# Optimization experiments

Hardware: AMD Instinct MI355X
Metric: run time of the kernel (lower is better)

The kernel has to match this reference:

```python
import jax, jax.numpy as jnp
import numpy as np

B, H, W = 64, 14, 14
DIM, NH, LORA = 768, 12, 4
HD = DIM // NH  # 64


def setup_inputs() -> dict:
    key = jax.random.key(0)
    ks = jax.random.split(key, 12)
    s = 0.02
    return {
        "x": jax.random.normal(ks[0], (B, H, W, DIM), dtype=jnp.float32),
        "qkv_w": jax.random.normal(ks[1], (3 * DIM, DIM), dtype=jnp.float32) * s,
        "qkv_b": jax.random.normal(ks[2], (3 * DIM,), dtype=jnp.float32) * s,
        "proj_w": jax.random.normal(ks[3], (DIM, DIM), dtype=jnp.float32) * s,
        "proj_b": jax.random.normal(ks[4], (DIM,), dtype=jnp.float32) * s,
        "la_q": jax.random.normal(ks[5], (LORA, DIM), dtype=jnp.float32) * s,
        "lb_q": jax.random.normal(ks[6], (DIM, LORA), dtype=jnp.float32) * s,
        "la_v": jax.random.normal(ks[7], (LORA, DIM), dtype=jnp.float32) * s,
        "lb_v": jax.random.normal(ks[8], (DIM, LORA), dtype=jnp.float32) * s,
        "rel_pos_h": jax.random.normal(ks[9], (2 * H - 1, HD), dtype=jnp.float32) * s,
        "rel_pos_w": jax.random.normal(ks[10], (2 * W - 1, HD), dtype=jnp.float32) * s,
    }


def reference(x, qkv_w, qkv_b, proj_w, proj_b, la_q, lb_q, la_v, lb_v, rel_pos_h, rel_pos_w):
    b, h, w, c = x.shape
    nh, hd = NH, c // NH
    scale = hd ** -0.5

    # qkv projection with LoRA deltas on q and v
    qkv = x @ qkv_w.T + qkv_b                       # (b,h,w,3c)
    new_q = (x @ la_q.T) @ lb_q.T                   # (b,h,w,c)
    new_v = (x @ la_v.T) @ lb_v.T
    qkv = qkv.at[..., :c].add(new_q)
    qkv = qkv.at[..., 2 * c:].add(new_v)

    qkv = qkv.reshape(b, h * w, 3, nh, hd).transpose(2, 0, 3, 1, 4)
    qkv = qkv.reshape(3, b * nh, h * w, hd)
    q, k, v = qkv[0], qkv[1], qkv[2]

    attn = jnp.einsum('bqd,bkd->bqk', q * scale, k)  # (b*nh, hw, hw)

    # decomposed relative position bias; q_size == k_size so no interpolation
    idx_h = jnp.arange(h)[:, None] - jnp.arange(h)[None, :] + (h - 1)
    idx_w = jnp.arange(w)[:, None] - jnp.arange(w)[None, :] + (w - 1)
    Rh = rel_pos_h[idx_h]                            # (h,h,hd)
    Rw = rel_pos_w[idx_w]                            # (w,w,hd)
    r_q = q.reshape(b * nh, h, w, hd)
    rel_h = jnp.einsum('bhwc,hkc->bhwk', r_q, Rh)    # (b*nh,h,w,h)
    rel_w = jnp.einsum('bhwc,wkc->bhwk', r_q, Rw)    # (b*nh,h,w,w)
    attn = (attn.reshape(b * nh, h, w, h, w)
            + rel_h[:, :, :, :, None]
            + rel_w[:, :, :, None, :]).reshape(b * nh, h * w, h * w)

    attn = jax.nn.softmax(attn, axis=-1)
    out = jnp.einsum('bqk,bkd->bqd', attn, v)        # (b*nh, hw, hd)
    out = out.reshape(b, nh, h, w, hd).transpose(0, 2, 3, 1, 4).reshape(b, h, w, c)
    return out @ proj_w.T + proj_b
```

## Files before the change

### kernel.cpp

```cpp
#include <hip/hip_runtime.h>
#include <stdint.h>

#define DIM   768
#define NH    12
#define HD    64
#define NT    196
#define M_ROWS 12544

typedef __attribute__((ext_vector_type(8))) short bf16x8;
typedef __attribute__((ext_vector_type(4))) float f32x4;

__device__ __forceinline__ float b2f(short s) {
  union { unsigned u; float f; } c;
  c.u = ((unsigned)(unsigned short)s) << 16;
  return c.f;
}
__device__ __forceinline__ short f2b(float f) {
  union { float f; unsigned u; } c; c.f = f;
  unsigned u = c.u;
  u += 0x7fffu + ((u >> 16) & 1u);
  return (short)(u >> 16);
}

__device__ __forceinline__ f32x4 mfma16(bf16x8 a, bf16x8 b, f32x4 c) {
  return __builtin_amdgcn_mfma_f32_16x16x32_bf16(a, b, c, 0, 0, 0);
}

__device__ __forceinline__ void g2lds16(const short* g, short* l) {
  __builtin_amdgcn_global_load_lds(
      (const __attribute__((address_space(1))) void*)g,
      (__attribute__((address_space(3))) void*)l, 16, 0, 0);
}

struct CvtArgs { const float* src[5]; int n4[5]; int off[5]; };

__global__ __launch_bounds__(256) void k_cvt(CvtArgs a, short* __restrict__ dst) {
  const int tid = blockIdx.x * 256 + threadIdx.x;
  const int stride = gridDim.x * 256;
  #pragma unroll
  for (int s = 0; s < 5; ++s) {
    const float4* sp = (const float4*)a.src[s];
    short4* dp = (short4*)(dst + a.off[s]);
    const int n4 = a.n4[s];
    for (int i = tid; i < n4; i += stride) {
      float4 v = sp[i];
      short4 o = { f2b(v.x), f2b(v.y), f2b(v.z), f2b(v.w) };
      dp[i] = o;
    }
  }
}

__global__ __launch_bounds__(256) void k_lora_xa(
    const float* __restrict__ x, const float* __restrict__ la_q,
    const float* __restrict__ la_v, float* __restrict__ xa)
{
  __shared__ float sla[8][DIM];
  const int tid = threadIdx.x;
  for (int i = tid; i < 8 * DIM; i += 256) {
    int j = i / DIM, c = i - j * DIM;
    sla[j][c] = (j < 4) ? la_q[j * DIM + c] : la_v[(j - 4) * DIM + c];
  }
  __syncthreads();
  const int lane = tid & 63, wid = tid >> 6;
  const int m = blockIdx.x * 4 + wid;
  const float4* xr = (const float4*)(x + (size_t)m * DIM);
  float s[8] = {};
  #pragma unroll
  for (int i = 0; i < 3; ++i) {
    float4 xv = xr[lane + 64 * i];
    int c = (lane + 64 * i) * 4;
    #pragma unroll
    for (int j = 0; j < 8; ++j)
      s[j] += xv.x * sla[j][c] + xv.y * sla[j][c + 1]
            + xv.z * sla[j][c + 2] + xv.w * sla[j][c + 3];
  }
  #pragma unroll
  for (int j = 0; j < 8; ++j) {
    #pragma unroll
    for (int off = 32; off; off >>= 1) s[j] += __shfl_xor(s[j], off);
  }
  if (lane == 0) {
    float* o = xa + m * 8;
    #pragma unroll
    for (int j = 0; j < 8; ++j) o[j] = s[j];
  }
}

template<int EPI>
__global__ __launch_bounds__(256) void k_gemm(
    const short* __restrict__ A, const short* __restrict__ B,
    const float* __restrict__ bias, const float* __restrict__ xa,
    const float* __restrict__ lb_q, const float* __restrict__ lb_v,
    short* __restrict__ out, float* __restrict__ outf)
{
  constexpr int K = DIM;
  __shared__ short sA[128 * 32];
  __shared__ short sB[128 * 32];
  const int tid = threadIdx.x, lane = tid & 63, wid = tid >> 6;
  const int rm0 = blockIdx.x * 128, cn0 = blockIdx.y * 128;
  const int wm = (wid >> 1) * 64, wn = (wid & 1) * 64;
  const int fr = lane & 15, fg = lane >> 4;
  f32x4 acc[4][4] = {};
  const short* ga = A + (size_t)(rm0 + (tid >> 2)) * K + (tid & 3) * 8;
  const short* gb = B + (size_t)(cn0 + (tid >> 2)) * K + (tid & 3) * 8;
  short* lA = sA + wid * 512;
  short* lB = sB + wid * 512;

  for (int kt = 0; kt < K; kt += 32) {
    g2lds16(ga + kt, lA);
    g2lds16(ga + 64 * K + kt, lA + 2048);
    g2lds16(gb + kt, lB);
    g2lds16(gb + 64 * K + kt, lB + 2048);
    __syncthreads();
    bf16x8 af[4], bg[4];
    #pragma unroll
    for (int i = 0; i < 4; ++i)
      af[i] = *(const bf16x8*)&sA[(wm + i * 16 + fr) * 32 + fg * 8];
    #pragma unroll
    for (int j = 0; j < 4; ++j)
      bg[j] = *(const bf16x8*)&sB[(wn + j * 16 + fr) * 32 + fg * 8];
    #pragma unroll
    for (int i = 0; i < 4; ++i)
      #pragma unroll
      for (int j = 0; j < 4; ++j)
        acc[i][j] = mfma16(af[i], bg[j], acc[i][j]);
    __syncthreads();
  }

  int ncol[4]; float biasv[4];
  #pragma unroll
  for (int j = 0; j < 4; ++j) {
    ncol[j] = cn0 + wn + j * 16 + fr;
    biasv[j] = bias[ncol[j]];
  }

  if (EPI == 0) {
    const int reg = cn0 / DIM;
    float lb[4][4];
    if (reg != 1) {
      const float* lbt = (reg == 0) ? lb_q : lb_v;
      #pragma unroll
      for (int j = 0; j < 4; ++j) {
        int ni = ncol[j] - reg * DIM;
        #pragma unroll
        for (int l = 0; l < 4; ++l) lb[j][l] = lbt[ni * 4 + l];
      }
    }
    #pragma unroll
    for (int i = 0; i < 4; ++i) {
      #pragma unroll
      for (int r = 0; r < 4; ++r) {
        int m = rm0 + wm + i * 16 + fg * 4 + r;
        int b_i = m / NT, p = m - b_i * NT;
        float xv0 = 0, xv1 = 0, xv2 = 0, xv3 = 0;
        if (reg != 1) {
          const float* xp = xa + m * 8 + (reg == 2 ? 4 : 0);
          xv0 = xp[0]; xv1 = xp[1]; xv2 = xp[2]; xv3 = xp[3];
        }
        #pragma unroll
        for (int j = 0; j < 4; ++j) {
          float val = acc[i][j][r] + biasv[j];
          if (reg != 1)
            val += xv0 * lb[j][0] + xv1 * lb[j][1] + xv2 * lb[j][2] + xv3 * lb[j][3];
          int ni = ncol[j] - reg * DIM;
          int head = ni >> 6, d = ni & 63;
          out[(size_t)reg * (M_ROWS * DIM)
              + ((size_t)(b_i * NH + head) * NT + p) * HD + d] = f2b(val);
        }
      }
    }
  } else {
    #pragma unroll
    for (int i = 0; i < 4; ++i)
      #pragma unroll
      for (int r = 0; r < 4; ++r) {
        int m = rm0 + wm + i * 16 + fg * 4 + r;
        #pragma unroll
        for (int j = 0; j < 4; ++j)
          outf[(size_t)m * DIM + ncol[j]] = acc[i][j][r] + biasv[j];
      }
  }
}

__global__ __launch_bounds__(256) void k_attn(
    const short* __restrict__ qb, const short* __restrict__ kb,
    const short* __restrict__ vb, const short* __restrict__ rph,
    const short* __restrict__ rpw, short* __restrict__ ao)
{
  __shared__ short vst[64][216];
  __shared__ short pwb[4][16][208];
  __shared__ short relh[NT * 14];
  __shared__ short relw[NT * 14];
  const int tid = threadIdx.x, lane = tid & 63, wid = tid >> 6;
  const int fr = lane & 15, fg = lane >> 4;
  const int bh = blockIdx.x;
  const int b_i = bh / NH, head = bh - b_i * NH;
  const short* q0 = qb + (size_t)bh * NT * HD;
  const short* k0 = kb + (size_t)bh * NT * HD;
  const short* v0 = vb + (size_t)bh * NT * HD;

  for (int i = tid; i < 64 * 20; i += 256) {
    int d = i / 20, c = 196 + (i - (i / 20) * 20);
    vst[d][c] = 0;
  }
  for (int t = tid; t < NT * 8; t += 256) {
    int p = t >> 3, d0 = (t & 7) * 8;
    bf16x8 vv = *(const bf16x8*)(v0 + p * HD + d0);
    #pragma unroll
    for (int j = 0; j < 8; ++j) vst[d0 + j][p] = vv[j];
  }
  for (int job = wid; job < 28; job += 4) {
    const int isW = job >= 14 ? 1 : 0;
    const int fx = isW ? job - 14 : job;
    const int qrow = isW ? fr * 14 + fx : fx * 14 + fr;
    const bool aok = fr < 14;
    const short* rp = isW ? rpw : rph;
    int ridx = fx - fr + 13;
    ridx = ridx < 0 ? 0 : (ridx > 26 ? 26 : ridx);
    f32x4 racc = {0.f, 0.f, 0.f, 0.f};
    #pragma unroll
    for (int ks = 0; ks < 2; ++ks) {
      bf16x8 afr = {0,0,0,0,0,0,0,0};
      if (aok) afr = *(const bf16x8*)(q0 + qrow * HD + ks * 32 + fg * 8);
      bf16x8 bfr = *(const bf16x8*)(rp + ridx * HD + ks * 32 + fg * 8);
      racc = mfma16(afr, bfr, racc);
    }
    #pragma unroll
    for (int r = 0; r < 4; ++r) {
      int rr = fg * 4 + r;
      if (rr < 14 && fr < 14) {
        int p = isW ? rr * 14 + fx : fx * 14 + rr;
        (isW ? relw : relh)[p * 14 + fr] = f2b(racc[r]);
      }
    }
  }
  __syncthreads();

  const float scale = 0.125f;
  for (int t = wid; t < 13; t += 4) {
    const int m0 = t * 16;
    bf16x8 aq0 = {0,0,0,0,0,0,0,0}, aq1 = {0,0,0,0,0,0,0,0};
    {
      int arow = m0 + fr;
      if (arow < NT) {
        aq0 = *(const bf16x8*)(q0 + arow * HD + fg * 8);
        aq1 = *(const bf16x8*)(q0 + arow * HD + 32 + fg * 8);
      }
    }
    f32x4 sc[13] = {};
    #pragma unroll
    for (int ct = 0; ct < 13; ++ct) {
      int brow = ct * 16 + fr;
      bf16x8 bk0 = {0,0,0,0,0,0,0,0}, bk1 = {0,0,0,0,0,0,0,0};
      if (brow < NT) {
        bk0 = *(const bf16x8*)(k0 + brow * HD + fg * 8);
        bk1 = *(const bf16x8*)(k0 + brow * HD + 32 + fg * 8);
      }
      sc[ct] = mfma16(aq0, bk0, sc[ct]);
      sc[ct] = mfma16(aq1, bk1, sc[ct]);
    }
    float rmax[4] = {-1e30f, -1e30f, -1e30f, -1e30f};
    #pragma unroll
    for (int ct = 0; ct < 13; ++ct) {
      int kk = ct * 16 + fr;
      int kh = kk / 14, kw = kk - kh * 14;
      #pragma unroll
      for (int r = 0; r < 4; ++r) {
        int p = m0 + fg * 4 + r;
        float v;
        if (kk < NT && p < NT)
          v = sc[ct][r] * scale + b2f(relh[p * 14 + kh]) + b2f(relw[p * 14 + kw]);
        else
          v = -1e30f;
        sc[ct][r] = v;
        rmax[r] = fmaxf(rmax[r], v);
      }
    }
    #pragma unroll
    for (int r = 0; r < 4; ++r) {
      rmax[r] = fmaxf(rmax[r], __shfl_xor(rmax[r], 1));
      rmax[r] = fmaxf(rmax[r], __shfl_xor(rmax[r], 2));
      rmax[r] = fmaxf(rmax[r], __shfl_xor(rmax[r], 4));
      rmax[r] = fmaxf(rmax[r], __shfl_xor(rmax[r], 8));
    }
    float rsum[4] = {0.f, 0.f, 0.f, 0.f};
    #pragma unroll
    for (int ct = 0; ct < 13; ++ct)
      #pragma unroll
      for (int r = 0; r < 4; ++r) {
        float e = __expf(sc[ct][r] - rmax[r]);
        sc[ct][r] = e;
        rsum[r] += e;
      }
    #pragma unroll
    for (int r = 0; r < 4; ++r) {
      rsum[r] += __shfl_xor(rsum[r], 1);
      rsum[r] += __shfl_xor(rsum[r], 2);
      rsum[r] += __shfl_xor(rsum[r], 4);
      rsum[r] += __shfl_xor(rsum[r], 8);
    }
    #pragma unroll
    for (int ct = 0; ct < 13; ++ct)
      #pragma unroll
      for (int r = 0; r < 4; ++r)
        pwb[wid][fg * 4 + r][ct * 16 + fr] = f2b(sc[ct][r]);

    f32x4 oacc[4] = {};
    #pragma unroll
    for (int ks = 0; ks < 7; ++ks) {
      const bool hi = (ks == 6) && (fg >= 2);
      bf16x8 pa = {0,0,0,0,0,0,0,0};
      if (!hi) pa = *(const bf16x8*)&pwb[wid][fr][ks * 32 + fg * 8];
      #pragma unroll
      for (int dt = 0; dt < 4; ++dt) {
        bf16x8 vv = {0,0,0,0,0,0,0,0};
        if (!hi) vv = *(const bf16x8*)&vst[dt * 16 + fr][ks * 32 + fg * 8];
        oacc[dt] = mfma16(pa, vv, oacc[dt]);
      }
    }
    #pragma unroll
    for (int r = 0; r < 4; ++r) {
      int p = m0 + fg * 4 + r;
      if (p < NT) {
        float inv = 1.0f / rsum[r];
        size_t base = ((size_t)(b_i * NT + p)) * DIM + head * HD;
        #pragma unroll
        for (int dt = 0; dt < 4; ++dt)
          ao[base + dt * 16 + fr] = f2b(oacc[dt][r] * inv);
      }
    }
  }
}

extern "C" void kernel_launch(void* const* d_in, const int* in_sizes, int n_in,
                              void* d_out, int out_size, void* d_ws, size_t ws_size,
                              hipStream_t stream) {
  const float *x = nullptr, *qkv_w = nullptr, *qkv_b = nullptr,
              *proj_w = nullptr, *proj_b = nullptr, *rph = nullptr,
              *rpw = nullptr;
  const float* c3072[4] = {nullptr, nullptr, nullptr, nullptr};
  int n3072 = 0, n1728 = 0;
  for (int i = 0; i < n_in; ++i) {
    const float* p = (const float*)d_in[i];
    switch (in_sizes[i]) {
      case 9633792: x = p; break;
      case 1769472: qkv_w = p; break;
      case 2304:    qkv_b = p; break;
      case 589824:  proj_w = p; break;
      case 768:     proj_b = p; break;
      case 3072:    if (n3072 < 4) c3072[n3072++] = p; break;
      case 1728:    { if (n1728 == 0) rph = p; else rpw = p; ++n1728; } break;
      default: break;
    }
  }
  const bool alpha = (n_in >= 1 && in_sizes[n_in - 1] == 9633792);
  const float* la_q = c3072[0];
  const float* lb_q = alpha ? c3072[2] : c3072[1];
  const float* la_v = alpha ? c3072[1] : c3072[2];
  const float* lb_v = c3072[3];

  float* out = (float*)d_out;

  char* ws = (char*)d_ws;
  float* xa   = (float*)ws;
  short* qkvb = (short*)(ws + 401408);
  short* q_   = qkvb;
  short* k_   = qkvb + (size_t)M_ROWS * DIM;
  short* v_   = qkvb + (size_t)2 * M_ROWS * DIM;
  short* cvt  = (short*)(ws + 401408 + 57802752);
  short* xb      = cvt;
  short* qkv_wb  = cvt + 9633792;
  short* proj_wb = cvt + 11403264;
  short* rphb    = cvt + 11993088;
  short* rpwb    = cvt + 11994816;
  short* ao = xb;

  CvtArgs ca;
  ca.src[0] = x;      ca.n4[0] = 9633792 / 4;  ca.off[0] = 0;
  ca.src[1] = qkv_w;  ca.n4[1] = 1769472 / 4;  ca.off[1] = 9633792;
  ca.src[2] = proj_w; ca.n4[2] =  589824 / 4;  ca.off[2] = 11403264;
  ca.src[3] = rph;    ca.n4[3] =    1728 / 4;  ca.off[3] = 11993088;
  ca.src[4] = rpw;    ca.n4[4] =    1728 / 4;  ca.off[4] = 11994816;

  k_cvt<<<1024, 256, 0, stream>>>(ca, cvt);
  k_lora_xa<<<3136, 256, 0, stream>>>(x, la_q, la_v, xa);
  k_gemm<0><<<dim3(98, 18), 256, 0, stream>>>(xb, qkv_wb, qkv_b, xa, lb_q, lb_v,
                                              qkvb, nullptr);
  k_attn<<<768, 256, 0, stream>>>(q_, k_, v_, rphb, rpwb, ao);
  k_gemm<1><<<dim3(98, 6), 256, 0, stream>>>(ao, proj_wb, proj_b, nullptr, nullptr,
                                             nullptr, nullptr, out);
}
```

Measured before the change: 206.7 us.

## Fuse x bf16 conversion into LoRA kernel, swizzle GEMM LDS, remap blocks per XCD

The fp32-to-bf16 conversion of x now happens inside the LoRA down-projection kernel, which already reads every row of x, so x is read from global memory once instead of twice. The GEMM kernels get an XOR swizzle on the LDS layout (applied on both the global-to-LDS writes and the fragment reads) to reduce bank conflicts. They also use a 1D grid remapped so consecutive output tiles land on the same XCD for better L2 reuse. The weight conversion kernel shrinks to four sources and 512 blocks.

Measured after the change: 193.4 us. -6.4%, faster.

```diff
diff --git a/kernel.cpp b/kernel.cpp
--- a/kernel.cpp
+++ b/kernel.cpp
@@ -32,13 +32,13 @@
       (__attribute__((address_space(3))) void*)l, 16, 0, 0);
 }
 
-struct CvtArgs { const float* src[5]; int n4[5]; int off[5]; };
+struct CvtArgs { const float* src[4]; int n4[4]; int off[4]; };
 
 __global__ __launch_bounds__(256) void k_cvt(CvtArgs a, short* __restrict__ dst) {
   const int tid = blockIdx.x * 256 + threadIdx.x;
   const int stride = gridDim.x * 256;
   #pragma unroll
-  for (int s = 0; s < 5; ++s) {
+  for (int s = 0; s < 4; ++s) {
     const float4* sp = (const float4*)a.src[s];
     short4* dp = (short4*)(dst + a.off[s]);
     const int n4 = a.n4[s];
@@ -52,7 +52,8 @@
 
 __global__ __launch_bounds__(256) void k_lora_xa(
     const float* __restrict__ x, const float* __restrict__ la_q,
-    const float* __restrict__ la_v, float* __restrict__ xa)
+    const float* __restrict__ la_v, float* __restrict__ xa,
+    short* __restrict__ xb)
 {
   __shared__ float sla[8][DIM];
   const int tid = threadIdx.x;
@@ -64,10 +65,13 @@
   const int lane = tid & 63, wid = tid >> 6;
   const int m = blockIdx.x * 4 + wid;
   const float4* xr = (const float4*)(x + (size_t)m * DIM);
+  short4* xbr = (short4*)(xb + (size_t)m * DIM);
   float s[8] = {};
   #pragma unroll
   for (int i = 0; i < 3; ++i) {
     float4 xv = xr[lane + 64 * i];
+    short4 o = { f2b(xv.x), f2b(xv.y), f2b(xv.z), f2b(xv.w) };
+    xbr[lane + 64 * i] = o;
     int c = (lane + 64 * i) * 4;
     #pragma unroll
     for (int j = 0; j < 8; ++j)
@@ -86,7 +90,7 @@
   }
 }
 
-template<int EPI>
+template<int EPI, int NCOL>
 __global__ __launch_bounds__(256) void k_gemm(
     const short* __restrict__ A, const short* __restrict__ B,
     const float* __restrict__ bias, const float* __restrict__ xa,
@@ -94,17 +98,30 @@
     short* __restrict__ out, float* __restrict__ outf)
 {
   constexpr int K = DIM;
-  __shared__ short sA[128 * 32];
-  __shared__ short sB[128 * 32];
+  constexpr int NWG = 98 * NCOL;
+  constexpr int Q = NWG / 8, R = NWG % 8;
+  __shared__ short sA[4096];
+  __shared__ short sB[4096];
+
+  const int g = blockIdx.x;
+  const int xcd = g & 7, idx = g >> 3;
+  const int wgid = (xcd < R) ? xcd * (Q + 1) + idx
+                             : R * (Q + 1) + (xcd - R) * Q + idx;
+  const int rm0 = (wgid / NCOL) * 128;
+  const int cn0 = (wgid % NCOL) * 128;
+
   const int tid = threadIdx.x, lane = tid & 63, wid = tid >> 6;
-  const int rm0 = blockIdx.x * 128, cn0 = blockIdx.y * 128;
   const int wm = (wid >> 1) * 64, wn = (wid & 1) * 64;
   const int fr = lane & 15, fg = lane >> 4;
   f32x4 acc[4][4] = {};
-  const short* ga = A + (size_t)(rm0 + (tid >> 2)) * K + (tid & 3) * 8;
-  const short* gb = B + (size_t)(cn0 + (tid >> 2)) * K + (tid & 3) * 8;
+
+  const int r_ = tid >> 2;
+  const int s_ = (tid & 3) ^ ((tid >> 3) & 3);
+  const short* ga = A + (size_t)(rm0 + r_) * K + s_ * 8;
+  const short* gb = B + (size_t)(cn0 + r_) * K + s_ * 8;
   short* lA = sA + wid * 512;
   short* lB = sB + wid * 512;
+  const int swz8 = (fg ^ ((fr >> 1) & 3)) * 8;
 
   for (int kt = 0; kt < K; kt += 32) {
     g2lds16(ga + kt, lA);
@@ -115,10 +132,10 @@
     bf16x8 af[4], bg[4];
     #pragma unroll
     for (int i = 0; i < 4; ++i)
-      af[i] = *(const bf16x8*)&sA[(wm + i * 16 + fr) * 32 + fg * 8];
+      af[i] = *(const bf16x8*)&sA[(wm + i * 16 + fr) * 32 + swz8];
     #pragma unroll
     for (int j = 0; j < 4; ++j)
-      bg[j] = *(const bf16x8*)&sB[(wn + j * 16 + fr) * 32 + fg * 8];
+      bg[j] = *(const bf16x8*)&sB[(wn + j * 16 + fr) * 32 + swz8];
     #pragma unroll
     for (int i = 0; i < 4; ++i)
       #pragma unroll
@@ -376,17 +393,16 @@
   short* ao = xb;
 
   CvtArgs ca;
-  ca.src[0] = x;      ca.n4[0] = 9633792 / 4;  ca.off[0] = 0;
-  ca.src[1] = qkv_w;  ca.n4[1] = 1769472 / 4;  ca.off[1] = 9633792;
-  ca.src[2] = proj_w; ca.n4[2] =  589824 / 4;  ca.off[2] = 11403264;
-  ca.src[3] = rph;    ca.n4[3] =    1728 / 4;  ca.off[3] = 11993088;
-  ca.src[4] = rpw;    ca.n4[4] =    1728 / 4;  ca.off[4] = 11994816;
-
-  k_cvt<<<1024, 256, 0, stream>>>(ca, cvt);
-  k_lora_xa<<<3136, 256, 0, stream>>>(x, la_q, la_v, xa);
-  k_gemm<0><<<dim3(98, 18), 256, 0, stream>>>(xb, qkv_wb, qkv_b, xa, lb_q, lb_v,
-                                              qkvb, nullptr);
+  ca.src[0] = qkv_w;  ca.n4[0] = 1769472 / 4;  ca.off[0] = 9633792;
+  ca.src[1] = proj_w; ca.n4[1] =  589824 / 4;  ca.off[1] = 11403264;
+  ca.src[2] = rph;    ca.n4[2] =    1728 / 4;  ca.off[2] = 11993088;
+  ca.src[3] = rpw;    ca.n4[3] =    1728 / 4;  ca.off[3] = 11994816;
+
+  k_cvt<<<512, 256, 0, stream>>>(ca, cvt);
+  k_lora_xa<<<3136, 256, 0, stream>>>(x, la_q, la_v, xa, xb);
+  k_gemm<0, 18><<<98 * 18, 256, 0, stream>>>(xb, qkv_wb, qkv_b, xa, lb_q, lb_v,
+                                             qkvb, nullptr);
   k_attn<<<768, 256, 0, stream>>>(q_, k_, v_, rphb, rpwb, ao);
-  k_gemm<1><<<dim3(98, 6), 256, 0, stream>>>(ao, proj_wb, proj_b, nullptr, nullptr,
-                                             nullptr, nullptr, out);
-}
+  k_gemm<1, 6><<<98 * 6, 256, 0, stream>>>(ao, proj_wb, proj_b, nullptr, nullptr,
+                                           nullptr, nullptr, out);
+}
```
